# Performance work log

Hardware: AMD Instinct MI355X
Metric: run time of the kernel (lower is better)

## Reference

```python
import jax, jax.numpy as jnp
import numpy as np

_ICO_FACES0 = [
    [0,11,5],[0,5,1],[0,1,7],[0,7,10],[0,10,11],
    [1,5,9],[5,11,4],[11,10,2],[10,7,6],[7,1,8],
    [3,9,4],[3,4,2],[3,2,6],[3,6,8],[3,8,9],
    [4,9,5],[2,4,11],[6,2,10],[8,6,7],[9,8,1]]


def ico_sphere_np(level=1):
    t = (1.0 + 5.0 ** 0.5) / 2.0
    verts = np.array([[-1,t,0],[1,t,0],[-1,-t,0],[1,-t,0],
                      [0,-1,t],[0,1,t],[0,-1,-t],[0,1,-t],
                      [t,0,-1],[t,0,1],[-t,0,-1],[-t,0,1]], dtype=np.float64)
    verts = verts / np.linalg.norm(verts, axis=1, keepdims=True)
    faces = [list(f) for f in _ICO_FACES0]
    for _ in range(level):
        vlist = [v for v in verts]
        cache = {}
        def mid(a, b):
            k = (min(a, b), max(a, b))
            if k not in cache:
                v = vlist[a] + vlist[b]
                vlist.append(v / np.linalg.norm(v))
                cache[k] = len(vlist) - 1
            return cache[k]
        nf = []
        for a, b, c in faces:
            ab, bc, ca = mid(a, b), mid(b, c), mid(c, a)
            nf += [[a, ab, ca], [b, bc, ab], [c, ca, bc], [ab, bc, ca]]
        faces = nf
        verts = np.stack(vlist)
    return verts.astype(np.float32), np.array(faces, dtype=np.int32)


def make_template():
    verts, faces = ico_sphere_np(1)          # (42,3), (80,3)
    v = verts[None]                          # (1,42,3)
    vmin = v.min(axis=1, keepdims=True)
    vmax = v.max(axis=1, keepdims=True)
    center = (vmin + vmax) / 2.0
    scale = (vmax - vmin).max() / 2.0        # normalize_to_box
    tv = 1.4 * (v - center) / scale          # cage_size = 1.4
    return jnp.asarray(np.transpose(tv, (0, 2, 1))), jnp.asarray(faces)  # (1,3,42),(80,3)


def optimize_cage(cage, shape, distance=0.4, iters=100, step=0.01):
    # cage (1,3,C), shape (B,3,N)
    B = shape.shape[0]
    cage = jnp.broadcast_to(cage, (B,) + cage.shape[1:])
    def body(_, c):
        d = jnp.sqrt(jnp.sum((c[:, :, :, None] - shape[:, :, None, :]) ** 2, axis=1))  # (B,C,N)
        min_d = jnp.min(d, axis=2)                                                     # (B,C)
        upd = (min_d > distance).astype(c.dtype)
        return c + step * (-c) * upd[:, None, :]
    return jax.lax.fori_loop(0, iters, body, cage)


def mean_value_coordinates_3D(query, vertices, faces):
    # query (B,P,3), vertices (B,C,3), faces (F,3) shared across batch
    B, P, _ = query.shape
    C = vertices.shape[1]
    r1 = jnp.array([1, 2, 0]); r2 = jnp.array([2, 0, 1])
    uj = vertices[:, None] - query[:, :, None]            # (B,P,C,3)
    dj = jnp.linalg.norm(uj, axis=-1, keepdims=True)      # (B,P,C,1)
    uj = uj / dj
    ui = uj[:, :, faces]                                  # (B,P,F,3,3)
    li = jnp.linalg.norm(ui[:, :, :, r1] - ui[:, :, :, r2], axis=-1)  # (B,P,F,3)
    eps = 2e-5
    li = jnp.where(li >= 2, li - jax.lax.stop_gradient(li - (2 - eps)), li)
    li = jnp.where(li <= -2, li - jax.lax.stop_gradient(li + (2 - eps)), li)
    theta = 2.0 * jnp.arcsin(li / 2.0)                    # (B,P,F,3)
    h = jnp.sum(theta, axis=-1, keepdims=True) / 2.0      # (B,P,F,1)
    ci = 2.0 * jnp.sin(h) * jnp.sin(h - theta) / (jnp.sin(theta[..., r1]) * jnp.sin(theta[..., r2])) - 1.0
    ci = jnp.clip(ci, -1 + 1e-5, 1 - 1e-5)
    si = jnp.sign(jnp.linalg.det(ui))[..., None] * jnp.sqrt(1.0 - ci ** 2)  # (B,P,F,3)
    di = dj[..., 0][:, :, faces]                          # (B,P,F,3)
    wi = (theta - ci[..., r1] * theta[..., r2] - ci[..., r2] * theta[..., r1]) / (di * jnp.sin(theta[..., r1]) * si[..., r2])
    inside = (jnp.pi - h[..., 0]) < 1e-4                  # (B,P,F)
    any_inside = jnp.any(inside, axis=-1, keepdims=True)[..., None]  # (B,P,1,1)
    wi = jnp.where(any_inside, 0.0, wi)
    wi = jnp.where(inside[..., None], jnp.sin(theta) * di[..., r2] * di[..., r1], wi)
    # scatter face corners -> vertices (B,P,F*3) -> (B,P,C)
    wj = jnp.zeros((B, P, C), wi.dtype).at[:, :, faces.reshape(-1)].add(wi.reshape(B, P, -1))
    close = dj[..., 0] < 1e-8                             # (B,P,C)
    wj = jnp.where(jnp.any(close, axis=-1, keepdims=True), 0.0, wj)
    wj = jnp.where(close, 1.0, wj)
    sumWj = jnp.sum(wj, axis=-1, keepdims=True)
    sumWj = jnp.where(sumWj == 0, 1.0, sumWj)
    return wj / sumWj, wi


def setup_inputs() -> dict:
    key = jax.random.key(0)
    ks = jax.random.split(key, 12)
    B, N, FEAT = 16, 8192, 256
    template_vertices, faces = make_template()
    def lin(k, fi, fo):
        k1, k2 = jax.random.split(k)
        return (jax.random.normal(k1, (fi, fo), jnp.float32) / np.sqrt(fi).astype(np.float32),
                jax.random.normal(k2, (fo,), jnp.float32) * 0.01)
    W1, b1 = lin(ks[0], 2 * FEAT, 512)
    W2, b2 = lin(ks[1], 512, 512)
    W3, b3 = lin(ks[2], 512, 256)
    W4, b4 = lin(ks[3], 256, 42 * 3)
    return {
        'source_shape': jax.random.normal(ks[4], (B, 3, N), jnp.float32),
        'target_shape': jax.random.normal(ks[5], (B, 3, N), jnp.float32),
        'source_f': jax.random.normal(ks[6], (B, FEAT), jnp.float32),
        'target_f': jax.random.normal(ks[7], (B, FEAT), jnp.float32),
        'template_vertices': template_vertices, 'faces': faces,
        'W1': W1, 'b1': b1, 'W2': W2, 'b2': b2, 'W3': W3, 'b3': b3, 'W4': W4, 'b4': b4,
    }


def reference(source_shape, target_shape, source_f, target_f, template_vertices, faces,
              W1, b1, W2, b2, W3, b3, W4, b4):
    B = source_shape.shape[0]
    cage = optimize_cage(template_vertices, source_shape)        # (B,3,42)
    feat = jnp.concatenate([source_f, target_f], axis=-1)        # (B,512)
    h = jax.nn.relu(feat @ W1 + b1)
    h = jax.nn.relu(h @ W2 + b2)
    h = jax.nn.relu(h @ W3 + b3)
    influence_offset = h @ W4 + b4                               # (B,126)
    cage_offset = influence_offset.reshape(B, 3, -1)             # (B,3,42)
    new_cage = cage + cage_offset
    cage_t = jnp.transpose(cage, (0, 2, 1))                      # (B,42,3)
    new_cage_t = jnp.transpose(new_cage, (0, 2, 1))
    weights, _ = mean_value_coordinates_3D(jnp.transpose(source_shape, (0, 2, 1)), cage_t, faces)
    weights = jax.lax.stop_gradient(weights)                     # weights.detach() in deform_with_MVC
    deformed = jnp.einsum('bpc,bcd->bpd', weights, new_cage_t)   # (B,N,3)
    return cage_t, new_cage_t, jnp.transpose(deformed, (0, 2, 1)), weights, influence_offset
```

## Files before the change

kernel.cpp:

```cpp
#include <hip/hip_runtime.h>
#include <math.h>

#define BB 16
#define NP 8192
#define NV 42
#define NF 80
#define FEAT 256
#define PPB 64
#define FH  40
#define WJS 65

__device__ __forceinline__ float rcp_f(float x)  { return __builtin_amdgcn_rcpf(x); }
__device__ __forceinline__ float rsq_f(float x)  { return __builtin_amdgcn_rsqf(x); }
__device__ __forceinline__ float sqrt_f(float x) { return __builtin_amdgcn_sqrtf(x); }

__device__ __forceinline__ float theta_from_x(float x) {
  bool big = x > 0.5f;
  float z = big ? fmaf(-0.5f, x, 0.5f) : x * x;
  float s = big ? sqrt_f(z) : x;
  float P = fmaf(z, 0.022371875f, 0.030381944f);
  P = fmaf(z, P, 0.044642857f);
  P = fmaf(z, P, 0.075f);
  P = fmaf(z, P, 0.16666667f);
  float r = fmaf(s * z, P, s);
  return big ? fmaf(-4.f, r, 3.14159265358979f) : 2.f * r;
}

__device__ __attribute__((noinline)) void inside_face_rt(
    int f0, int f1, int f2, const float4* vpos,
    float qx, float qy, float qz, float* wjh)
{
  float4 v0 = vpos[f0], v1 = vpos[f1], v2 = vpos[f2];
  float a0x = v0.x - qx, a0y = v0.y - qy, a0z = v0.z - qz;
  float a1x = v1.x - qx, a1y = v1.y - qy, a1z = v1.z - qz;
  float a2x = v2.x - qx, a2y = v2.y - qy, a2z = v2.z - qz;
  float ss0 = fmaf(a0x, a0x, fmaf(a0y, a0y, a0z * a0z));
  float ss1 = fmaf(a1x, a1x, fmaf(a1y, a1y, a1z * a1z));
  float ss2 = fmaf(a2x, a2x, fmaf(a2y, a2y, a2z * a2z));
  float i0 = rsq_f(ss0), i1 = rsq_f(ss1), i2 = rsq_f(ss2);
  float d0 = ss0 * i0, d1 = ss1 * i1, d2 = ss2 * i2;
  float u0x = a0x * i0, u0y = a0y * i0, u0z = a0z * i0;
  float u1x = a1x * i1, u1y = a1y * i1, u1z = a1z * i1;
  float u2x = a2x * i2, u2y = a2y * i2, u2z = a2z * i2;
  float ex = u1x - u2x, ey = u1y - u2y, ez = u1z - u2z;
  float x0 = 0.5f * sqrt_f(fmaf(ex, ex, fmaf(ey, ey, ez * ez)));
  ex = u2x - u0x; ey = u2y - u0y; ez = u2z - u0z;
  float x1 = 0.5f * sqrt_f(fmaf(ex, ex, fmaf(ey, ey, ez * ez)));
  ex = u0x - u1x; ey = u0y - u1y; ez = u0z - u1z;
  float x2 = 0.5f * sqrt_f(fmaf(ex, ex, fmaf(ey, ey, ez * ez)));
  if (x0 >= 1.f) x0 = 0.99999f;
  if (x1 >= 1.f) x1 = 0.99999f;
  if (x2 >= 1.f) x2 = 0.99999f;
  float th0 = theta_from_x(x0), th1 = theta_from_x(x1), th2 = theta_from_x(x2);
  float hh = 0.5f * ((th0 + th1) + th2);
  if (3.14159265358979f - hh < 1e-4f) {
    float cx0 = sqrt_f(fmaxf(fmaf(-x0, x0, 1.f), 0.f));
    float cx1 = sqrt_f(fmaxf(fmaf(-x1, x1, 1.f), 0.f));
    float cx2 = sqrt_f(fmaxf(fmaf(-x2, x2, 1.f), 0.f));
    wjh[f0 * WJS] += (2.f * (x0 * cx0) * d2) * d1;
    wjh[f1 * WJS] += (2.f * (x1 * cx1) * d0) * d2;
    wjh[f2 * WJS] += (2.f * (x2 * cx2) * d1) * d0;
  }
}

__global__ __launch_bounds__(128) void mvc_kernel(
    const float* __restrict__ src,
    const float* __restrict__ cage_t,
    const float* __restrict__ ncage_t,
    const int* __restrict__ faces,
    float* __restrict__ out_def,
    float* __restrict__ out_w)
{
  __shared__ float4 vpos[NV];
  __shared__ float4 npos[NV];
  __shared__ int fidp[NF];
  __shared__ float wj[2 * NV * WJS];
  __shared__ unsigned long long closeM[2][PPB];
  __shared__ int insideF[2][PPB];

  const float PI_F = 3.14159265358979323846f;
  int tid = threadIdx.x;
  int p   = tid & (PPB - 1);
  int hf  = tid >> 6;
  int b    = blockIdx.x / (NP / PPB);
  int pblk = blockIdx.x % (NP / PPB);
  int gp   = pblk * PPB + p;

  if (tid < NV) {
    const float* cp = cage_t + (size_t)b * NV * 3 + tid * 3;
    vpos[tid] = make_float4(cp[0], cp[1], cp[2], 0.f);
    const float* np_ = ncage_t + (size_t)b * NV * 3 + tid * 3;
    npos[tid] = make_float4(np_[0], np_[1], np_[2], 0.f);
  }
  if (tid < NF) {
    int f0 = faces[3 * tid], f1 = faces[3 * tid + 1], f2 = faces[3 * tid + 2];
    fidp[tid] = f0 | (f1 << 6) | (f2 << 12);
  }
  for (int i = tid; i < 2 * NV * WJS; i += 128) wj[i] = 0.f;
  __syncthreads();

  float qx = src[(size_t)b * 3 * NP + gp];
  float qy = src[(size_t)b * 3 * NP + NP + gp];
  float qz = src[(size_t)b * 3 * NP + 2 * NP + gp];

  int anyInside = 0;
  unsigned long long closeMask = 0ull;
  float* wjh = wj + hf * (NV * WJS) + p;

  #pragma unroll 2
  for (int i = hf * FH; i < hf * FH + FH; i++) {
    int pk = fidp[i];
    int f0 = pk & 63, f1 = (pk >> 6) & 63, f2 = pk >> 12;
    float4 v0 = vpos[f0], v1 = vpos[f1], v2 = vpos[f2];
    float a0x = v0.x - qx, a0y = v0.y - qy, a0z = v0.z - qz;
    float a1x = v1.x - qx, a1y = v1.y - qy, a1z = v1.z - qz;
    float a2x = v2.x - qx, a2y = v2.y - qy, a2z = v2.z - qz;
    float ss0 = fmaf(a0x, a0x, fmaf(a0y, a0y, a0z * a0z));
    float ss1 = fmaf(a1x, a1x, fmaf(a1y, a1y, a1z * a1z));
    float ss2 = fmaf(a2x, a2x, fmaf(a2y, a2y, a2z * a2z));
    if (ss0 < 1e-16f) closeMask |= (1ull << f0);
    if (ss1 < 1e-16f) closeMask |= (1ull << f1);
    if (ss2 < 1e-16f) closeMask |= (1ull << f2);
    float i0 = rsq_f(ss0), i1 = rsq_f(ss1), i2 = rsq_f(ss2);
    float d0 = ss0 * i0, d1 = ss1 * i1, d2 = ss2 * i2;
    float u0x = a0x * i0, u0y = a0y * i0, u0z = a0z * i0;
    float u1x = a1x * i1, u1y = a1y * i1, u1z = a1z * i1;
    float u2x = a2x * i2, u2y = a2y * i2, u2z = a2z * i2;
    float ex = u1x - u2x, ey = u1y - u2y, ez = u1z - u2z;
    float x0 = 0.5f * sqrt_f(fmaf(ex, ex, fmaf(ey, ey, ez * ez)));
    ex = u2x - u0x; ey = u2y - u0y; ez = u2z - u0z;
    float x1 = 0.5f * sqrt_f(fmaf(ex, ex, fmaf(ey, ey, ez * ez)));
    ex = u0x - u1x; ey = u0y - u1y; ez = u0z - u1z;
    float x2 = 0.5f * sqrt_f(fmaf(ex, ex, fmaf(ey, ey, ez * ez)));
    if (x0 >= 1.f) x0 = 0.99999f;
    if (x1 >= 1.f) x1 = 0.99999f;
    if (x2 >= 1.f) x2 = 0.99999f;
    float cx0 = sqrt_f(fmaxf(fmaf(-x0, x0, 1.f), 0.f));
    float cx1 = sqrt_f(fmaxf(fmaf(-x1, x1, 1.f), 0.f));
    float cx2 = sqrt_f(fmaxf(fmaf(-x2, x2, 1.f), 0.f));
    float th0 = theta_from_x(x0);
    float th1 = theta_from_x(x1);
    float th2 = theta_from_x(x2);
    float hh = 0.5f * ((th0 + th1) + th2);
    if (PI_F - hh < 1e-4f) anyInside = 1;
    float t0 = x0 * cx0, t1 = x1 * cx1, t2 = x2 * cx2;
    float st0 = t0 + t0, st1 = t1 + t1, st2 = t2 + t2;
    float A1 = x0 * (cx1 * cx2);
    float A2 = x1 * (cx0 * cx2);
    float A3 = x2 * (cx0 * cx1);
    float A4 = x0 * (x1 * x2);
    float sh  = ((A1 + A2) + A3) - A4;
    float sm0 = ((-A1 + A2) + A3) + A4;
    float sm1 = ((A1 - A2) + A3) + A4;
    float sm2 = ((A1 + A2) - A3) + A4;
    float twosh = sh + sh;
    float c0 = fmaf(twosh * sm0, rcp_f(st1 * st2), -1.f);
    float c1 = fmaf(twosh * sm1, rcp_f(st2 * st0), -1.f);
    float c2 = fmaf(twosh * sm2, rcp_f(st0 * st1), -1.f);
    c0 = fminf(fmaxf(c0, -0.99999f), 0.99999f);
    c1 = fminf(fmaxf(c1, -0.99999f), 0.99999f);
    c2 = fminf(fmaxf(c2, -0.99999f), 0.99999f);
    float det = u0x * fmaf(u1y, u2z, -(u1z * u2y))
              - u0y * fmaf(u1x, u2z, -(u1z * u2x))
              + u0z * fmaf(u1x, u2y, -(u1y * u2x));
    float sg = (det > 0.f) ? 1.f : ((det < 0.f) ? -1.f : 0.f);
    float sn0 = sg * sqrt_f(fmaf(-c0, c0, 1.f));
    float sn1 = sg * sqrt_f(fmaf(-c1, c1, 1.f));
    float sn2 = sg * sqrt_f(fmaf(-c2, c2, 1.f));
    float w0 = fmaf(-c2, th1, fmaf(-c1, th2, th0)) * rcp_f((d0 * st1) * sn2);
    float w1 = fmaf(-c0, th2, fmaf(-c2, th0, th1)) * rcp_f((d1 * st2) * sn0);
    float w2 = fmaf(-c1, th0, fmaf(-c0, th1, th2)) * rcp_f((d2 * st0) * sn1);
    wjh[f0 * WJS] += w0;
    wjh[f1 * WJS] += w1;
    wjh[f2 * WJS] += w2;
  }

  closeM[hf][p]  = closeMask;
  insideF[hf][p] = anyInside;
  __syncthreads();

  int mIn = insideF[0][p] | insideF[1][p];
  unsigned long long mCl = closeM[0][p] | closeM[1][p];

  if (mIn) {
    for (int c = 0; c < NV; c++) wjh[c * WJS] = 0.f;
    #pragma unroll 1
    for (int i = hf * FH; i < hf * FH + FH; i++) {
      int pk = fidp[i];
      inside_face_rt(pk & 63, (pk >> 6) & 63, pk >> 12, vpos, qx, qy, qz, wjh);
    }
  }
  __syncthreads();

  if (tid < PPB) {
    float sum = 0.f;
    for (int c = 0; c < NV; c++) {
      float w = wj[c * WJS + p] + wj[(NV + c) * WJS + p];
      if (mCl) w = ((mCl >> c) & 1ull) ? 1.f : 0.f;
      wj[c * WJS + p] = w;
      sum += w;
    }
    if (sum == 0.f) sum = 1.f;
    float inv = rcp_f(sum);
    float ax = 0.f, ay = 0.f, az = 0.f;
    for (int c = 0; c < NV; c++) {
      float w = wj[c * WJS + p] * inv;
      wj[c * WJS + p] = w;
      float4 n = npos[c];
      ax = fmaf(w, n.x, ax);
      ay = fmaf(w, n.y, ay);
      az = fmaf(w, n.z, az);
    }
    out_def[(size_t)b * 3 * NP + gp]          = ax;
    out_def[(size_t)b * 3 * NP + NP + gp]     = ay;
    out_def[(size_t)b * 3 * NP + 2 * NP + gp] = az;
  }
  __syncthreads();

  float* wbase = out_w + ((size_t)b * NP + pblk * PPB) * NV;
  for (int idx = tid; idx < PPB * NV; idx += 128) {
    int pp = idx / NV;
    int c  = idx - pp * NV;
    wbase[idx] = wj[c * WJS + pp];
  }
}

__device__ __forceinline__ void splitk_body(
    const float* in0, const float* in1,
    const float* W, const float* bias, float* out,
    int FI, int FO, int relu, int ox, int bb, int tid,
    float* sIn, float (*part)[64])
{
  for (int i = tid; i < FI; i += 256) {
    float v;
    if (in1) v = (i < FEAT) ? in0[(size_t)bb * FEAT + i]
                            : in1[(size_t)bb * FEAT + i - FEAT];
    else     v = in0[(size_t)bb * FI + i];
    sIn[i] = v;
  }
  __syncthreads();
  int o = ox * 64 + (tid & 63);
  int kk = tid >> 6;
  int seg = FI >> 2;
  float acc = 0.f;
  const float* wp = W + o;
  #pragma unroll 4
  for (int i = kk * seg; i < (kk + 1) * seg; i++)
    acc = fmaf(sIn[i], wp[(size_t)i * FO], acc);
  part[kk][tid & 63] = acc;
  __syncthreads();
  if (tid < 64) {
    float r = ((part[0][tid] + part[1][tid]) + (part[2][tid] + part[3][tid]))
              + bias[o];
    out[(size_t)bb * FO + o] = relu ? fmaxf(r, 0.f) : r;
  }
}

__global__ __launch_bounds__(256) void cage_l1_kernel(
    const float* __restrict__ tmpl, const float* __restrict__ src,
    const float* __restrict__ sf, const float* __restrict__ tf,
    const float* __restrict__ W1, const float* __restrict__ b1,
    float* __restrict__ cage, float* __restrict__ h1)
{
  __shared__ float red[8];
  __shared__ float sIn[512];
  __shared__ float part[4][64];
  int tid = threadIdx.x;

  if (blockIdx.x < BB * NV) {
    int b = blockIdx.x / NV;
    int v = blockIdx.x % NV;
    const float* sp = src + (size_t)b * 3 * NP;
    float cx = tmpl[v], cy = tmpl[NV + v], cz = tmpl[2 * NV + v];
    int k = 0;
    while (true) {
      float m = 3.4e38f;
      for (int i = tid; i < NP; i += 256) {
        float dx = __fsub_rn(cx, sp[i]);
        float dy = __fsub_rn(cy, sp[NP + i]);
        float dz = __fsub_rn(cz, sp[2 * NP + i]);
        float ss = __fadd_rn(__fadd_rn(__fmul_rn(dx, dx), __fmul_rn(dy, dy)),
                             __fmul_rn(dz, dz));
        m = fminf(m, ss);
      }
      #pragma unroll
      for (int off = 32; off > 0; off >>= 1)
        m = fminf(m, __shfl_down(m, off, 64));
      int wid = tid >> 6;
      __syncthreads();
      if ((tid & 63) == 0) red[wid] = m;
      __syncthreads();
      if (tid == 0) {
        float mm = fminf(fminf(red[0], red[1]), fminf(red[2], red[3]));
        red[4] = sqrtf(mm);
      }
      __syncthreads();
      float mind = red[4];
      if (mind > 0.4f && k < 100) {
        cx = __fsub_rn(cx, __fmul_rn(0.01f, cx));
        cy = __fsub_rn(cy, __fmul_rn(0.01f, cy));
        cz = __fsub_rn(cz, __fmul_rn(0.01f, cz));
        k++;
      } else {
        break;
      }
    }
    if (tid == 0) {
      cage[(size_t)b * 3 * NV + v]          = cx;
      cage[(size_t)b * 3 * NV + NV + v]     = cy;
      cage[(size_t)b * 3 * NV + 2 * NV + v] = cz;
    }
  } else {
    int idx = blockIdx.x - BB * NV;
    splitk_body(sf, tf, W1, b1, h1, 512, 512, 1, idx & 7, idx >> 3,
                tid, sIn, part);
  }
}

__global__ __launch_bounds__(256) void linear_splitk(
    const float* __restrict__ in0, const float* __restrict__ in1,
    const float* __restrict__ W, const float* __restrict__ bias,
    float* __restrict__ out, int FI, int FO, int relu)
{
  __shared__ float sIn[512];
  __shared__ float part[4][64];
  splitk_body(in0, in1, W, bias, out, FI, FO, relu,
              blockIdx.x, blockIdx.y, threadIdx.x, sIn, part);
}

__global__ __launch_bounds__(128) void l4_finalize_kernel(
    const float* __restrict__ h3,
    const float* __restrict__ W4, const float* __restrict__ b4,
    const float* __restrict__ cage,
    float* __restrict__ out_io,
    float* __restrict__ cage_t,
    float* __restrict__ ncage_t)
{
  __shared__ float sIn[256];
  int bb = blockIdx.x;
  int tid = threadIdx.x;
  sIn[tid] = h3[(size_t)bb * 256 + tid];
  sIn[tid + 128] = h3[(size_t)bb * 256 + tid + 128];
  __syncthreads();
  if (tid < 126) {
    float acc = b4[tid];
    const float* wp = W4 + tid;
    #pragma unroll 4
    for (int i = 0; i < 256; i++) acc = fmaf(sIn[i], wp[(size_t)i * 126], acc);
    out_io[(size_t)bb * 126 + tid] = acc;
    float c  = cage[(size_t)bb * 126 + tid];
    float nc = c + acc;
    int d = tid / NV, v = tid - d * NV;
    cage_t[(size_t)bb * NV * 3 + v * 3 + d]  = c;
    ncage_t[(size_t)bb * NV * 3 + v * 3 + d] = nc;
  }
}

extern "C" void kernel_launch(void* const* d_in, const int* in_sizes, int n_in,
                              void* d_out, int out_size, void* d_ws, size_t ws_size,
                              hipStream_t stream) {
  (void)in_sizes; (void)n_in; (void)out_size; (void)d_ws; (void)ws_size;
  const float* src   = (const float*)d_in[0];
  const float* sf    = (const float*)d_in[2];
  const float* tf    = (const float*)d_in[3];
  const float* tmpl  = (const float*)d_in[4];
  const int*   faces = (const int*)d_in[5];
  const float* W1 = (const float*)d_in[6];  const float* b1 = (const float*)d_in[7];
  const float* W2 = (const float*)d_in[8];  const float* b2 = (const float*)d_in[9];
  const float* W3 = (const float*)d_in[10]; const float* b3 = (const float*)d_in[11];
  const float* W4 = (const float*)d_in[12]; const float* b4 = (const float*)d_in[13];

  float* out = (float*)d_out;
  float* out_cage_t  = out;
  float* out_ncage_t = out + 2016;
  float* out_def     = out + 4032;
  float* out_w       = out + 397248;
  float* out_io      = out + 5902272;

  float* s_cage = out_w;
  float* s_h1   = out_w + 2016;
  float* s_h2   = out_w + 10208;
  float* s_h3   = out_w + 18400;

  cage_l1_kernel<<<dim3(BB * NV + 128), dim3(256), 0, stream>>>(
      tmpl, src, sf, tf, W1, b1, s_cage, s_h1);
  linear_splitk<<<dim3(8, BB), dim3(256), 0, stream>>>(s_h1, nullptr, W2, b2, s_h2, 512, 512, 1);
  linear_splitk<<<dim3(4, BB), dim3(256), 0, stream>>>(s_h2, nullptr, W3, b3, s_h3, 512, 256, 1);
  l4_finalize_kernel<<<dim3(BB), dim3(128), 0, stream>>>(
      s_h3, W4, b4, s_cage, out_io, out_cage_t, out_ncage_t);
  mvc_kernel<<<dim3(BB * (NP / PPB)), dim3(128), 0, stream>>>(
      src, out_cage_t, out_ncage_t, faces, out_def, out_w);
}
```

Baseline: 165.1 us.

## Give each wave its own points in MVC and fuse MLP layers 2-4 into one kernel

The MVC kernel now assigns 64 distinct points to each wave, and each wave loops over all 80 faces. This removes the cross-half reduction of partial weights and close/inside flags through shared memory, along with two block barriers. Separately, layers 2-4 of the MLP are merged into a single per-batch kernel, dropping two launches and the intermediate global buffers. The trade-off is that the fused MLP runs on only 16 blocks that each stream the full weight matrices, and the MVC kernel has half as many threads working on each point.

```diff
diff --git a/kernel.cpp b/kernel.cpp
--- a/kernel.cpp
+++ b/kernel.cpp
@@ -6,8 +6,7 @@
 #define NV 42
 #define NF 80
 #define FEAT 256
-#define PPB 64
-#define FH  40
+#define PPW 64
 #define WJS 65
 
 __device__ __forceinline__ float rcp_f(float x)  { return __builtin_amdgcn_rcpf(x); }
@@ -74,17 +73,15 @@
   __shared__ float4 vpos[NV];
   __shared__ float4 npos[NV];
   __shared__ int fidp[NF];
-  __shared__ float wj[2 * NV * WJS];
-  __shared__ unsigned long long closeM[2][PPB];
-  __shared__ int insideF[2][PPB];
+  __shared__ float wj[2][NV * WJS];
 
   const float PI_F = 3.14159265358979323846f;
-  int tid = threadIdx.x;
-  int p   = tid & (PPB - 1);
-  int hf  = tid >> 6;
-  int b    = blockIdx.x / (NP / PPB);
-  int pblk = blockIdx.x % (NP / PPB);
-  int gp   = pblk * PPB + p;
+  int tid  = threadIdx.x;
+  int lane = tid & 63;
+  int wv   = tid >> 6;
+  int b    = blockIdx.x / (NP / 128);
+  int pblk = blockIdx.x % (NP / 128);
+  int gp   = pblk * 128 + wv * PPW + lane;
 
   if (tid < NV) {
     const float* cp = cage_t + (size_t)b * NV * 3 + tid * 3;
@@ -96,7 +93,7 @@
     int f0 = faces[3 * tid], f1 = faces[3 * tid + 1], f2 = faces[3 * tid + 2];
     fidp[tid] = f0 | (f1 << 6) | (f2 << 12);
   }
-  for (int i = tid; i < 2 * NV * WJS; i += 128) wj[i] = 0.f;
+  for (int i = tid; i < 2 * NV * WJS; i += 128) wj[0][i] = 0.f;
   __syncthreads();
 
   float qx = src[(size_t)b * 3 * NP + gp];
@@ -105,10 +102,10 @@
 
   int anyInside = 0;
   unsigned long long closeMask = 0ull;
-  float* wjh = wj + hf * (NV * WJS) + p;
-
-  #pragma unroll 2
-  for (int i = hf * FH; i < hf * FH + FH; i++) {
+  float* wjh = &wj[wv][lane];
+
+  #pragma unroll 1
+  for (int i = 0; i < NF; i++) {
     int pk = fidp[i];
     int f0 = pk & 63, f1 = (pk >> 6) & 63, f2 = pk >> 12;
     float4 v0 = vpos[f0], v1 = vpos[f1], v2 = vpos[f2];
@@ -175,37 +172,32 @@
     wjh[f2 * WJS] += w2;
   }
 
-  closeM[hf][p]  = closeMask;
-  insideF[hf][p] = anyInside;
-  __syncthreads();
-
-  int mIn = insideF[0][p] | insideF[1][p];
-  unsigned long long mCl = closeM[0][p] | closeM[1][p];
-
-  if (mIn) {
+  if (anyInside) {
     for (int c = 0; c < NV; c++) wjh[c * WJS] = 0.f;
     #pragma unroll 1
-    for (int i = hf * FH; i < hf * FH + FH; i++) {
+    for (int i = 0; i < NF; i++) {
       int pk = fidp[i];
       inside_face_rt(pk & 63, (pk >> 6) & 63, pk >> 12, vpos, qx, qy, qz, wjh);
     }
   }
-  __syncthreads();
-
-  if (tid < PPB) {
+
+  {
     float sum = 0.f;
-    for (int c = 0; c < NV; c++) {
-      float w = wj[c * WJS + p] + wj[(NV + c) * WJS + p];
-      if (mCl) w = ((mCl >> c) & 1ull) ? 1.f : 0.f;
-      wj[c * WJS + p] = w;
-      sum += w;
+    if (closeMask) {
+      for (int c = 0; c < NV; c++) {
+        float w = ((closeMask >> c) & 1ull) ? 1.f : 0.f;
+        wjh[c * WJS] = w;
+        sum += w;
+      }
+    } else {
+      for (int c = 0; c < NV; c++) sum += wjh[c * WJS];
     }
     if (sum == 0.f) sum = 1.f;
     float inv = rcp_f(sum);
     float ax = 0.f, ay = 0.f, az = 0.f;
     for (int c = 0; c < NV; c++) {
-      float w = wj[c * WJS + p] * inv;
-      wj[c * WJS + p] = w;
+      float w = wjh[c * WJS] * inv;
+      wjh[c * WJS] = w;
       float4 n = npos[c];
       ax = fmaf(w, n.x, ax);
       ay = fmaf(w, n.y, ay);
@@ -217,11 +209,11 @@
   }
   __syncthreads();
 
-  float* wbase = out_w + ((size_t)b * NP + pblk * PPB) * NV;
-  for (int idx = tid; idx < PPB * NV; idx += 128) {
+  float* wbase = out_w + ((size_t)b * NP + pblk * 128) * NV;
+  for (int idx = tid; idx < 128 * NV; idx += 128) {
     int pp = idx / NV;
     int c  = idx - pp * NV;
-    wbase[idx] = wj[c * WJS + pp];
+    wbase[idx] = wj[pp >> 6][c * WJS + (pp & 63)];
   }
 }
 
@@ -317,36 +309,49 @@
   }
 }
 
-__global__ __launch_bounds__(256) void linear_splitk(
-    const float* __restrict__ in0, const float* __restrict__ in1,
-    const float* __restrict__ W, const float* __restrict__ bias,
-    float* __restrict__ out, int FI, int FO, int relu)
-{
-  __shared__ float sIn[512];
-  __shared__ float part[4][64];
-  splitk_body(in0, in1, W, bias, out, FI, FO, relu,
-              blockIdx.x, blockIdx.y, threadIdx.x, sIn, part);
-}
-
-__global__ __launch_bounds__(128) void l4_finalize_kernel(
-    const float* __restrict__ h3,
+__global__ __launch_bounds__(256) void mlp_tail_kernel(
+    const float* __restrict__ h1,
+    const float* __restrict__ W2, const float* __restrict__ b2,
+    const float* __restrict__ W3, const float* __restrict__ b3,
     const float* __restrict__ W4, const float* __restrict__ b4,
     const float* __restrict__ cage,
     float* __restrict__ out_io,
     float* __restrict__ cage_t,
     float* __restrict__ ncage_t)
 {
-  __shared__ float sIn[256];
+  __shared__ float sA[512];
+  __shared__ float sB[512];
   int bb = blockIdx.x;
   int tid = threadIdx.x;
-  sIn[tid] = h3[(size_t)bb * 256 + tid];
-  sIn[tid + 128] = h3[(size_t)bb * 256 + tid + 128];
+  sA[tid]       = h1[(size_t)bb * 512 + tid];
+  sA[tid + 256] = h1[(size_t)bb * 512 + tid + 256];
+  __syncthreads();
+  {
+    int o0 = tid, o1 = tid + 256;
+    float a0 = b2[o0], a1 = b2[o1];
+    #pragma unroll 4
+    for (int i = 0; i < 512; i++) {
+      float s = sA[i];
+      a0 = fmaf(s, W2[(size_t)i * 512 + o0], a0);
+      a1 = fmaf(s, W2[(size_t)i * 512 + o1], a1);
+    }
+    sB[o0] = fmaxf(a0, 0.f);
+    sB[o1] = fmaxf(a1, 0.f);
+  }
+  __syncthreads();
+  {
+    float a0 = b3[tid];
+    #pragma unroll 4
+    for (int i = 0; i < 512; i++)
+      a0 = fmaf(sB[i], W3[(size_t)i * 256 + tid], a0);
+    sA[tid] = fmaxf(a0, 0.f);
+  }
   __syncthreads();
   if (tid < 126) {
     float acc = b4[tid];
     const float* wp = W4 + tid;
     #pragma unroll 4
-    for (int i = 0; i < 256; i++) acc = fmaf(sIn[i], wp[(size_t)i * 126], acc);
+    for (int i = 0; i < 256; i++) acc = fmaf(sA[i], wp[(size_t)i * 126], acc);
     out_io[(size_t)bb * 126 + tid] = acc;
     float c  = cage[(size_t)bb * 126 + tid];
     float nc = c + acc;
@@ -379,15 +384,11 @@
 
   float* s_cage = out_w;
   float* s_h1   = out_w + 2016;
-  float* s_h2   = out_w + 10208;
-  float* s_h3   = out_w + 18400;
 
   cage_l1_kernel<<<dim3(BB * NV + 128), dim3(256), 0, stream>>>(
       tmpl, src, sf, tf, W1, b1, s_cage, s_h1);
-  linear_splitk<<<dim3(8, BB), dim3(256), 0, stream>>>(s_h1, nullptr, W2, b2, s_h2, 512, 512, 1);
-  linear_splitk<<<dim3(4, BB), dim3(256), 0, stream>>>(s_h2, nullptr, W3, b3, s_h3, 512, 256, 1);
-  l4_finalize_kernel<<<dim3(BB), dim3(128), 0, stream>>>(
-      s_h3, W4, b4, s_cage, out_io, out_cage_t, out_ncage_t);
-  mvc_kernel<<<dim3(BB * (NP / PPB)), dim3(128), 0, stream>>>(
+  mlp_tail_kernel<<<dim3(BB), dim3(256), 0, stream>>>(
+      s_h1, W2, b2, W3, b3, W4, b4, s_cage, out_io, out_cage_t, out_ncage_t);
+  mvc_kernel<<<dim3(BB * (NP / 128)), dim3(128), 0, stream>>>(
       src, out_cage_t, out_ncage_t, faces, out_def, out_w);
 }
```

Result: slower. 202.3 us (+22.5%).

## Process two points per thread over all faces instead of splitting faces across halves

Applied to the files above, without the earlier changes.

The MVC kernel now has each thread handle two query points across all 80 faces, instead of two threads sharing one point with 40 faces each. This drops the cross-half reduction, the shared close/inside flags and a barrier. It also allows paired float2-style arithmetic that may map to packed FP32 instructions. The cost is four times fewer blocks (256 points per block), higher register pressure, a larger shared accumulation buffer, and per-point serialized inside-face fallback loops.

```diff
diff --git a/kernel.cpp b/kernel.cpp
--- a/kernel.cpp
+++ b/kernel.cpp
@@ -6,9 +6,7 @@
 #define NV 42
 #define NF 80
 #define FEAT 256
-#define PPB 64
-#define FH  40
-#define WJS 65
+#define WJS 129
 
 __device__ __forceinline__ float rcp_f(float x)  { return __builtin_amdgcn_rcpf(x); }
 __device__ __forceinline__ float rsq_f(float x)  { return __builtin_amdgcn_rsqf(x); }
@@ -26,11 +24,47 @@
   return big ? fmaf(-4.f, r, 3.14159265358979f) : 2.f * r;
 }
 
+struct f2 { float x, y; };
+__device__ __forceinline__ f2 mkf2(float a, float b) { f2 r; r.x = a; r.y = b; return r; }
+__device__ __forceinline__ f2 f2add(f2 a, f2 b) { return mkf2(a.x + b.x, a.y + b.y); }
+__device__ __forceinline__ f2 f2sub(f2 a, f2 b) { return mkf2(a.x - b.x, a.y - b.y); }
+__device__ __forceinline__ f2 f2subs(float s, f2 b) { return mkf2(s - b.x, s - b.y); }
+__device__ __forceinline__ f2 f2mul(f2 a, f2 b) { return mkf2(a.x * b.x, a.y * b.y); }
+__device__ __forceinline__ f2 f2muls(float s, f2 a) { return mkf2(s * a.x, s * a.y); }
+__device__ __forceinline__ f2 f2fma(f2 a, f2 b, f2 c) {
+  return mkf2(fmaf(a.x, b.x, c.x), fmaf(a.y, b.y, c.y));
+}
+__device__ __forceinline__ f2 f2neg(f2 a) { return mkf2(-a.x, -a.y); }
+__device__ __forceinline__ f2 f2rsq(f2 a) { return mkf2(rsq_f(a.x), rsq_f(a.y)); }
+__device__ __forceinline__ f2 f2rcp(f2 a) { return mkf2(rcp_f(a.x), rcp_f(a.y)); }
+__device__ __forceinline__ f2 f2sqrt(f2 a) { return mkf2(sqrt_f(a.x), sqrt_f(a.y)); }
+__device__ __forceinline__ f2 f2clampx(f2 a) {
+  return mkf2(a.x >= 1.f ? 0.99999f : a.x, a.y >= 1.f ? 0.99999f : a.y);
+}
+__device__ __forceinline__ f2 f2cx(f2 x) {
+  return mkf2(sqrt_f(fmaxf(fmaf(-x.x, x.x, 1.f), 0.f)),
+              sqrt_f(fmaxf(fmaf(-x.y, x.y, 1.f), 0.f)));
+}
+__device__ __forceinline__ f2 f2sq1mc(f2 c) {
+  return mkf2(sqrt_f(fmaf(-c.x, c.x, 1.f)), sqrt_f(fmaf(-c.y, c.y, 1.f)));
+}
+__device__ __forceinline__ f2 f2theta(f2 x) {
+  return mkf2(theta_from_x(x.x), theta_from_x(x.y));
+}
+__device__ __forceinline__ f2 f2clampc(f2 c) {
+  return mkf2(fminf(fmaxf(c.x, -0.99999f), 0.99999f),
+              fminf(fmaxf(c.y, -0.99999f), 0.99999f));
+}
+__device__ __forceinline__ f2 f2sign(f2 d) {
+  return mkf2((d.x > 0.f) ? 1.f : ((d.x < 0.f) ? -1.f : 0.f),
+              (d.y > 0.f) ? 1.f : ((d.y < 0.f) ? -1.f : 0.f));
+}
+
 __device__ __attribute__((noinline)) void inside_face_rt(
-    int f0, int f1, int f2, const float4* vpos,
+    int f0, int f1, int f2i, const float4* vpos,
     float qx, float qy, float qz, float* wjh)
 {
-  float4 v0 = vpos[f0], v1 = vpos[f1], v2 = vpos[f2];
+  float4 v0 = vpos[f0], v1 = vpos[f1], v2 = vpos[f2i];
   float a0x = v0.x - qx, a0y = v0.y - qy, a0z = v0.z - qz;
   float a1x = v1.x - qx, a1y = v1.y - qy, a1z = v1.z - qz;
   float a2x = v2.x - qx, a2y = v2.y - qy, a2z = v2.z - qz;
@@ -57,9 +91,9 @@
     float cx0 = sqrt_f(fmaxf(fmaf(-x0, x0, 1.f), 0.f));
     float cx1 = sqrt_f(fmaxf(fmaf(-x1, x1, 1.f), 0.f));
     float cx2 = sqrt_f(fmaxf(fmaf(-x2, x2, 1.f), 0.f));
-    wjh[f0 * WJS] += (2.f * (x0 * cx0) * d2) * d1;
-    wjh[f1 * WJS] += (2.f * (x1 * cx1) * d0) * d2;
-    wjh[f2 * WJS] += (2.f * (x2 * cx2) * d1) * d0;
+    wjh[f0 * WJS]  += (2.f * (x0 * cx0) * d2) * d1;
+    wjh[f1 * WJS]  += (2.f * (x1 * cx1) * d0) * d2;
+    wjh[f2i * WJS] += (2.f * (x2 * cx2) * d1) * d0;
   }
 }
 
@@ -74,17 +108,16 @@
   __shared__ float4 vpos[NV];
   __shared__ float4 npos[NV];
   __shared__ int fidp[NF];
-  __shared__ float wj[2 * NV * WJS];
-  __shared__ unsigned long long closeM[2][PPB];
-  __shared__ int insideF[2][PPB];
+  __shared__ float wj[2][NV * WJS];
 
   const float PI_F = 3.14159265358979323846f;
-  int tid = threadIdx.x;
-  int p   = tid & (PPB - 1);
-  int hf  = tid >> 6;
-  int b    = blockIdx.x / (NP / PPB);
-  int pblk = blockIdx.x % (NP / PPB);
-  int gp   = pblk * PPB + p;
+  int tid  = threadIdx.x;
+  int lane = tid & 63;
+  int wv   = tid >> 6;
+  int b    = blockIdx.x / (NP / 256);
+  int pblk = blockIdx.x % (NP / 256);
+  int gpA  = pblk * 256 + wv * 128 + lane;
+  int gpB  = gpA + 64;
 
   if (tid < NV) {
     const float* cp = cage_t + (size_t)b * NV * 3 + tid * 3;
@@ -93,119 +126,122 @@
     npos[tid] = make_float4(np_[0], np_[1], np_[2], 0.f);
   }
   if (tid < NF) {
-    int f0 = faces[3 * tid], f1 = faces[3 * tid + 1], f2 = faces[3 * tid + 2];
-    fidp[tid] = f0 | (f1 << 6) | (f2 << 12);
-  }
-  for (int i = tid; i < 2 * NV * WJS; i += 128) wj[i] = 0.f;
+    int f0 = faces[3 * tid], f1 = faces[3 * tid + 1], f2i = faces[3 * tid + 2];
+    fidp[tid] = f0 | (f1 << 6) | (f2i << 12);
+  }
+  for (int i = tid; i < 2 * NV * WJS; i += 128) wj[0][i] = 0.f;
   __syncthreads();
 
-  float qx = src[(size_t)b * 3 * NP + gp];
-  float qy = src[(size_t)b * 3 * NP + NP + gp];
-  float qz = src[(size_t)b * 3 * NP + 2 * NP + gp];
-
-  int anyInside = 0;
-  unsigned long long closeMask = 0ull;
-  float* wjh = wj + hf * (NV * WJS) + p;
-
-  #pragma unroll 2
-  for (int i = hf * FH; i < hf * FH + FH; i++) {
+  f2 qx = mkf2(src[(size_t)b * 3 * NP + gpA],          src[(size_t)b * 3 * NP + gpB]);
+  f2 qy = mkf2(src[(size_t)b * 3 * NP + NP + gpA],     src[(size_t)b * 3 * NP + NP + gpB]);
+  f2 qz = mkf2(src[(size_t)b * 3 * NP + 2 * NP + gpA], src[(size_t)b * 3 * NP + 2 * NP + gpB]);
+
+  int inA = 0, inB = 0;
+  unsigned long long clA = 0ull, clB = 0ull;
+  float* wjA = &wj[wv][lane];
+  float* wjB = wjA + 64;
+
+  #pragma unroll 1
+  for (int i = 0; i < NF; i++) {
     int pk = fidp[i];
-    int f0 = pk & 63, f1 = (pk >> 6) & 63, f2 = pk >> 12;
-    float4 v0 = vpos[f0], v1 = vpos[f1], v2 = vpos[f2];
-    float a0x = v0.x - qx, a0y = v0.y - qy, a0z = v0.z - qz;
-    float a1x = v1.x - qx, a1y = v1.y - qy, a1z = v1.z - qz;
-    float a2x = v2.x - qx, a2y = v2.y - qy, a2z = v2.z - qz;
-    float ss0 = fmaf(a0x, a0x, fmaf(a0y, a0y, a0z * a0z));
-    float ss1 = fmaf(a1x, a1x, fmaf(a1y, a1y, a1z * a1z));
-    float ss2 = fmaf(a2x, a2x, fmaf(a2y, a2y, a2z * a2z));
-    if (ss0 < 1e-16f) closeMask |= (1ull << f0);
-    if (ss1 < 1e-16f) closeMask |= (1ull << f1);
-    if (ss2 < 1e-16f) closeMask |= (1ull << f2);
-    float i0 = rsq_f(ss0), i1 = rsq_f(ss1), i2 = rsq_f(ss2);
-    float d0 = ss0 * i0, d1 = ss1 * i1, d2 = ss2 * i2;
-    float u0x = a0x * i0, u0y = a0y * i0, u0z = a0z * i0;
-    float u1x = a1x * i1, u1y = a1y * i1, u1z = a1z * i1;
-    float u2x = a2x * i2, u2y = a2y * i2, u2z = a2z * i2;
-    float ex = u1x - u2x, ey = u1y - u2y, ez = u1z - u2z;
-    float x0 = 0.5f * sqrt_f(fmaf(ex, ex, fmaf(ey, ey, ez * ez)));
-    ex = u2x - u0x; ey = u2y - u0y; ez = u2z - u0z;
-    float x1 = 0.5f * sqrt_f(fmaf(ex, ex, fmaf(ey, ey, ez * ez)));
-    ex = u0x - u1x; ey = u0y - u1y; ez = u0z - u1z;
-    float x2 = 0.5f * sqrt_f(fmaf(ex, ex, fmaf(ey, ey, ez * ez)));
-    if (x0 >= 1.f) x0 = 0.99999f;
-    if (x1 >= 1.f) x1 = 0.99999f;
-    if (x2 >= 1.f) x2 = 0.99999f;
-    float cx0 = sqrt_f(fmaxf(fmaf(-x0, x0, 1.f), 0.f));
-    float cx1 = sqrt_f(fmaxf(fmaf(-x1, x1, 1.f), 0.f));
-    float cx2 = sqrt_f(fmaxf(fmaf(-x2, x2, 1.f), 0.f));
-    float th0 = theta_from_x(x0);
-    float th1 = theta_from_x(x1);
-    float th2 = theta_from_x(x2);
-    float hh = 0.5f * ((th0 + th1) + th2);
-    if (PI_F - hh < 1e-4f) anyInside = 1;
-    float t0 = x0 * cx0, t1 = x1 * cx1, t2 = x2 * cx2;
-    float st0 = t0 + t0, st1 = t1 + t1, st2 = t2 + t2;
-    float A1 = x0 * (cx1 * cx2);
-    float A2 = x1 * (cx0 * cx2);
-    float A3 = x2 * (cx0 * cx1);
-    float A4 = x0 * (x1 * x2);
-    float sh  = ((A1 + A2) + A3) - A4;
-    float sm0 = ((-A1 + A2) + A3) + A4;
-    float sm1 = ((A1 - A2) + A3) + A4;
-    float sm2 = ((A1 + A2) - A3) + A4;
-    float twosh = sh + sh;
-    float c0 = fmaf(twosh * sm0, rcp_f(st1 * st2), -1.f);
-    float c1 = fmaf(twosh * sm1, rcp_f(st2 * st0), -1.f);
-    float c2 = fmaf(twosh * sm2, rcp_f(st0 * st1), -1.f);
-    c0 = fminf(fmaxf(c0, -0.99999f), 0.99999f);
-    c1 = fminf(fmaxf(c1, -0.99999f), 0.99999f);
-    c2 = fminf(fmaxf(c2, -0.99999f), 0.99999f);
-    float det = u0x * fmaf(u1y, u2z, -(u1z * u2y))
-              - u0y * fmaf(u1x, u2z, -(u1z * u2x))
-              + u0z * fmaf(u1x, u2y, -(u1y * u2x));
-    float sg = (det > 0.f) ? 1.f : ((det < 0.f) ? -1.f : 0.f);
-    float sn0 = sg * sqrt_f(fmaf(-c0, c0, 1.f));
-    float sn1 = sg * sqrt_f(fmaf(-c1, c1, 1.f));
-    float sn2 = sg * sqrt_f(fmaf(-c2, c2, 1.f));
-    float w0 = fmaf(-c2, th1, fmaf(-c1, th2, th0)) * rcp_f((d0 * st1) * sn2);
-    float w1 = fmaf(-c0, th2, fmaf(-c2, th0, th1)) * rcp_f((d1 * st2) * sn0);
-    float w2 = fmaf(-c1, th0, fmaf(-c0, th1, th2)) * rcp_f((d2 * st0) * sn1);
-    wjh[f0 * WJS] += w0;
-    wjh[f1 * WJS] += w1;
-    wjh[f2 * WJS] += w2;
-  }
-
-  closeM[hf][p]  = closeMask;
-  insideF[hf][p] = anyInside;
-  __syncthreads();
-
-  int mIn = insideF[0][p] | insideF[1][p];
-  unsigned long long mCl = closeM[0][p] | closeM[1][p];
-
-  if (mIn) {
-    for (int c = 0; c < NV; c++) wjh[c * WJS] = 0.f;
-    #pragma unroll 1
-    for (int i = hf * FH; i < hf * FH + FH; i++) {
+    int f0 = pk & 63, f1 = (pk >> 6) & 63, f2i = pk >> 12;
+    float4 v0 = vpos[f0], v1 = vpos[f1], v2 = vpos[f2i];
+    f2 a0x = f2subs(v0.x, qx), a0y = f2subs(v0.y, qy), a0z = f2subs(v0.z, qz);
+    f2 a1x = f2subs(v1.x, qx), a1y = f2subs(v1.y, qy), a1z = f2subs(v1.z, qz);
+    f2 a2x = f2subs(v2.x, qx), a2y = f2subs(v2.y, qy), a2z = f2subs(v2.z, qz);
+    f2 ss0 = f2fma(a0x, a0x, f2fma(a0y, a0y, f2mul(a0z, a0z)));
+    f2 ss1 = f2fma(a1x, a1x, f2fma(a1y, a1y, f2mul(a1z, a1z)));
+    f2 ss2 = f2fma(a2x, a2x, f2fma(a2y, a2y, f2mul(a2z, a2z)));
+    if (ss0.x < 1e-16f) clA |= (1ull << f0);
+    if (ss1.x < 1e-16f) clA |= (1ull << f1);
+    if (ss2.x < 1e-16f) clA |= (1ull << f2i);
+    if (ss0.y < 1e-16f) clB |= (1ull << f0);
+    if (ss1.y < 1e-16f) clB |= (1ull << f1);
+    if (ss2.y < 1e-16f) clB |= (1ull << f2i);
+    f2 i0 = f2rsq(ss0), i1 = f2rsq(ss1), i2 = f2rsq(ss2);
+    f2 d0 = f2mul(ss0, i0), d1 = f2mul(ss1, i1), d2 = f2mul(ss2, i2);
+    f2 u0x = f2mul(a0x, i0), u0y = f2mul(a0y, i0), u0z = f2mul(a0z, i0);
+    f2 u1x = f2mul(a1x, i1), u1y = f2mul(a1y, i1), u1z = f2mul(a1z, i1);
+    f2 u2x = f2mul(a2x, i2), u2y = f2mul(a2y, i2), u2z = f2mul(a2z, i2);
+    f2 ex = f2sub(u1x, u2x), ey = f2sub(u1y, u2y), ez = f2sub(u1z, u2z);
+    f2 x0 = f2muls(0.5f, f2sqrt(f2fma(ex, ex, f2fma(ey, ey, f2mul(ez, ez)))));
+    ex = f2sub(u2x, u0x); ey = f2sub(u2y, u0y); ez = f2sub(u2z, u0z);
+    f2 x1 = f2muls(0.5f, f2sqrt(f2fma(ex, ex, f2fma(ey, ey, f2mul(ez, ez)))));
+    ex = f2sub(u0x, u1x); ey = f2sub(u0y, u1y); ez = f2sub(u0z, u1z);
+    f2 x2 = f2muls(0.5f, f2sqrt(f2fma(ex, ex, f2fma(ey, ey, f2mul(ez, ez)))));
+    x0 = f2clampx(x0); x1 = f2clampx(x1); x2 = f2clampx(x2);
+    f2 cx0 = f2cx(x0), cx1 = f2cx(x1), cx2 = f2cx(x2);
+    f2 th0 = f2theta(x0), th1 = f2theta(x1), th2 = f2theta(x2);
+    f2 hh = f2muls(0.5f, f2add(f2add(th0, th1), th2));
+    if (PI_F - hh.x < 1e-4f) inA = 1;
+    if (PI_F - hh.y < 1e-4f) inB = 1;
+    f2 t0 = f2mul(x0, cx0), t1 = f2mul(x1, cx1), t2 = f2mul(x2, cx2);
+    f2 st0 = f2add(t0, t0), st1 = f2add(t1, t1), st2 = f2add(t2, t2);
+    f2 A1 = f2mul(x0, f2mul(cx1, cx2));
+    f2 A2 = f2mul(x1, f2mul(cx0, cx2));
+    f2 A3 = f2mul(x2, f2mul(cx0, cx1));
+    f2 A4 = f2mul(x0, f2mul(x1, x2));
+    f2 sh  = f2sub(f2add(f2add(A1, A2), A3), A4);
+    f2 sm0 = f2add(f2add(f2sub(A2, A1), A3), A4);
+    f2 sm1 = f2add(f2add(f2sub(A1, A2), A3), A4);
+    f2 sm2 = f2add(f2sub(f2add(A1, A2), A3), A4);
+    f2 twosh = f2add(sh, sh);
+    f2 none = mkf2(-1.f, -1.f);
+    f2 c0 = f2fma(f2mul(twosh, sm0), f2rcp(f2mul(st1, st2)), none);
+    f2 c1 = f2fma(f2mul(twosh, sm1), f2rcp(f2mul(st2, st0)), none);
+    f2 c2 = f2fma(f2mul(twosh, sm2), f2rcp(f2mul(st0, st1)), none);
+    c0 = f2clampc(c0); c1 = f2clampc(c1); c2 = f2clampc(c2);
+    f2 m0 = f2fma(u1y, u2z, f2neg(f2mul(u1z, u2y)));
+    f2 m1 = f2fma(u1x, u2z, f2neg(f2mul(u1z, u2x)));
+    f2 m2 = f2fma(u1x, u2y, f2neg(f2mul(u1y, u2x)));
+    f2 det = f2add(f2sub(f2mul(u0x, m0), f2mul(u0y, m1)), f2mul(u0z, m2));
+    f2 sg = f2sign(det);
+    f2 sn0 = f2mul(sg, f2sq1mc(c0));
+    f2 sn1 = f2mul(sg, f2sq1mc(c1));
+    f2 sn2 = f2mul(sg, f2sq1mc(c2));
+    f2 w0 = f2mul(f2fma(f2neg(c2), th1, f2fma(f2neg(c1), th2, th0)),
+                  f2rcp(f2mul(f2mul(d0, st1), sn2)));
+    f2 w1 = f2mul(f2fma(f2neg(c0), th2, f2fma(f2neg(c2), th0, th1)),
+                  f2rcp(f2mul(f2mul(d1, st2), sn0)));
+    f2 w2 = f2mul(f2fma(f2neg(c1), th0, f2fma(f2neg(c0), th1, th2)),
+                  f2rcp(f2mul(f2mul(d2, st0), sn1)));
+    wjA[f0 * WJS]  += w0.x;  wjB[f0 * WJS]  += w0.y;
+    wjA[f1 * WJS]  += w1.x;  wjB[f1 * WJS]  += w1.y;
+    wjA[f2i * WJS] += w2.x;  wjB[f2i * WJS] += w2.y;
+  }
+
+  if (inA) {
+    for (int c = 0; c < NV; c++) wjA[c * WJS] = 0.f;
+    for (int i = 0; i < NF; i++) {
       int pk = fidp[i];
-      inside_face_rt(pk & 63, (pk >> 6) & 63, pk >> 12, vpos, qx, qy, qz, wjh);
-    }
-  }
-  __syncthreads();
-
-  if (tid < PPB) {
+      inside_face_rt(pk & 63, (pk >> 6) & 63, pk >> 12, vpos, qx.x, qy.x, qz.x, wjA);
+    }
+  }
+  if (inB) {
+    for (int c = 0; c < NV; c++) wjB[c * WJS] = 0.f;
+    for (int i = 0; i < NF; i++) {
+      int pk = fidp[i];
+      inside_face_rt(pk & 63, (pk >> 6) & 63, pk >> 12, vpos, qx.y, qy.y, qz.y, wjB);
+    }
+  }
+
+  auto finish = [&](float* wjh, unsigned long long mCl, int gp) {
     float sum = 0.f;
-    for (int c = 0; c < NV; c++) {
-      float w = wj[c * WJS + p] + wj[(NV + c) * WJS + p];
-      if (mCl) w = ((mCl >> c) & 1ull) ? 1.f : 0.f;
-      wj[c * WJS + p] = w;
-      sum += w;
+    if (mCl) {
+      for (int c = 0; c < NV; c++) {
+        float w = ((mCl >> c) & 1ull) ? 1.f : 0.f;
+        wjh[c * WJS] = w;
+        sum += w;
+      }
+    } else {
+      for (int c = 0; c < NV; c++) sum += wjh[c * WJS];
     }
     if (sum == 0.f) sum = 1.f;
     float inv = rcp_f(sum);
     float ax = 0.f, ay = 0.f, az = 0.f;
     for (int c = 0; c < NV; c++) {
-      float w = wj[c * WJS + p] * inv;
-      wj[c * WJS + p] = w;
+      float w = wjh[c * WJS] * inv;
+      wjh[c * WJS] = w;
       float4 n = npos[c];
       ax = fmaf(w, n.x, ax);
       ay = fmaf(w, n.y, ay);
@@ -214,14 +250,16 @@
     out_def[(size_t)b * 3 * NP + gp]          = ax;
     out_def[(size_t)b * 3 * NP + NP + gp]     = ay;
     out_def[(size_t)b * 3 * NP + 2 * NP + gp] = az;
-  }
+  };
+  finish(wjA, clA, gpA);
+  finish(wjB, clB, gpB);
   __syncthreads();
 
-  float* wbase = out_w + ((size_t)b * NP + pblk * PPB) * NV;
-  for (int idx = tid; idx < PPB * NV; idx += 128) {
+  float* wbase = out_w + ((size_t)b * NP + pblk * 256) * NV;
+  for (int idx = tid; idx < 256 * NV; idx += 128) {
     int pp = idx / NV;
     int c  = idx - pp * NV;
-    wbase[idx] = wj[c * WJS + pp];
+    wbase[idx] = wj[pp >> 7][c * WJS + (pp & 127)];
   }
 }
 
@@ -388,6 +426,6 @@
   linear_splitk<<<dim3(4, BB), dim3(256), 0, stream>>>(s_h2, nullptr, W3, b3, s_h3, 512, 256, 1);
   l4_finalize_kernel<<<dim3(BB), dim3(128), 0, stream>>>(
       s_h3, W4, b4, s_cage, out_io, out_cage_t, out_ncage_t);
-  mvc_kernel<<<dim3(BB * (NP / PPB)), dim3(128), 0, stream>>>(
+  mvc_kernel<<<dim3(BB * (NP / 256)), dim3(128), 0, stream>>>(
       src, out_cage_t, out_ncage_t, faces, out_def, out_w);
 }
```

After: 259.0 us. 1.57x slower.
